# Performance work log

Hardware: AMD Instinct MI355X
Metric: run time of the kernel (lower is better)

Reference implementation:

```python
import jax, jax.numpy as jnp
import numpy as np

P = 2048  # number of problems


def _structure():
    # Symbols per problem alternate 128/384; questions per problem alternate 32/96.
    p = np.arange(P)
    S = np.where(p % 2 == 0, 128, 384).astype(np.int64)   # num_symbols per problem
    Q = np.where(p % 2 == 0, 32, 96).astype(np.int64)     # num_questions per problem
    cost_starts = np.concatenate([[0], np.cumsum(S)])[:-1]  # row starts into costs_flat
    prob_of_question = np.repeat(p, Q)                     # [T_Q] problem id of each question
    S_per_q = np.repeat(S, Q)                              # [T_Q] symbols per question
    TQ = S_per_q.shape[0]
    qs_segment = np.repeat(np.arange(TQ), S_per_q)         # [T_total] question id of each element
    q_elem_starts = np.concatenate([[0], np.cumsum(S_per_q)])[:-1]
    T = qs_segment.shape[0]
    # offset of each element within its question, then add that problem's cost row start
    offsets = np.arange(T) - np.repeat(q_elem_starts, S_per_q)
    starts_per_q = np.repeat(cost_starts, Q)
    cost_index = np.repeat(starts_per_q, S_per_q) + offsets  # tile_like gather indices
    return (cost_index.astype(np.int32), qs_segment.astype(np.int32),
            prob_of_question.astype(np.int32))


def setup_inputs() -> dict:
    key = jax.random.key(0)
    k1, k2, k3 = jax.random.split(key, 3)
    cost_index, qs_segment, prob_of_question = _structure()
    T = cost_index.shape[0]            # 41_943_040
    TS = (P // 2) * (128 + 384)        # 524_288
    occ_flat = jax.random.uniform(k1, (T,), dtype=jnp.float32)   # occurrence counts >= 0
    costs_flat = jax.random.normal(k2, (TS,), dtype=jnp.float32)  # symbol costs (weights)
    valid = jax.random.uniform(k3, (P,)) < 0.9                    # per-problem valid mask
    return {
        'occ_flat': occ_flat,
        'costs_flat': costs_flat,
        'valid': valid,
        'cost_index': jnp.asarray(cost_index),
        'qs_segment': jnp.asarray(qs_segment),
        'prob_of_question': jnp.asarray(prob_of_question),
    }


def reference(occ_flat, costs_flat, valid, cost_index, qs_segment, prob_of_question):
    # tile_like: broadcast each problem's costs to each of its questions (gather)
    # costs_to_logits: elementwise multiply + per-question reduce_sum
    # costs_decorated_to_logits: invalid problems' logits are 0 (scatter_nd into zeros)
    TQ = prob_of_question.shape[0]
    potentials = occ_flat * costs_flat[cost_index]             # [T_total]
    logits_q = jax.ops.segment_sum(potentials, qs_segment, num_segments=TQ)  # [T_Q]
    return jnp.where(valid[prob_of_question], logits_q, jnp.zeros((), logits_q.dtype))
```

## Files before the change

kernel.cpp:

```cpp
#include <hip/hip_runtime.h>
#include <hip/hip_bf16.h>


typedef float f4 __attribute__((ext_vector_type(4)));

__device__ __forceinline__ float dot4(f4 a, f4 b) {
    return a.x * b.x + a.y * b.y + a.z * b.z + a.w * b.w;
}

#define TQ_HALF 65536

__global__ __launch_bounds__(256)
void classifier_kernel(const float* __restrict__ occ,
                       const float* __restrict__ costs,
                       const void*  __restrict__ valid,
                       float* __restrict__ out) {
    const int hid   = (blockIdx.x * blockDim.x + threadIdx.x) >> 5;
    const int lane  = threadIdx.x & 31;
    const int flane = threadIdx.x & 63;

    unsigned int w = ((const unsigned int*)valid)[flane];
    const bool u8 = (__ballot(w > 1u) != 0ull);

    const int pair   = hid >> 7;
    const int within = hid & 127;
    const int pair2  = pair + (TQ_HALF >> 7);

    float s0, s1;
    int prob0, prob1;
    if (within < 32) {
        prob0 = 2 * pair;
        prob1 = 2 * pair2;
        const f4* o0 = (const f4*)(occ + 40960 * pair  + 128 * within);
        const f4* o1 = (const f4*)(occ + 40960 * pair2 + 128 * within);
        const f4* c0 = (const f4*)(costs + 512 * pair);
        const f4* c1 = (const f4*)(costs + 512 * pair2);
        f4 a0 = __builtin_nontemporal_load(&o0[lane]);
        f4 a1 = __builtin_nontemporal_load(&o1[lane]);
        f4 b0 = c0[lane];
        f4 b1 = c1[lane];
        s0 = dot4(a0, b0);
        s1 = dot4(a1, b1);
    } else {
        prob0 = 2 * pair + 1;
        prob1 = 2 * pair2 + 1;
        const f4* o0 = (const f4*)(occ + 40960 * pair  + 4096 + 384 * (within - 32));
        const f4* o1 = (const f4*)(occ + 40960 * pair2 + 4096 + 384 * (within - 32));
        const f4* c0 = (const f4*)(costs + 512 * pair  + 128);
        const f4* c1 = (const f4*)(costs + 512 * pair2 + 128);
        f4 a00 = __builtin_nontemporal_load(&o0[lane]);
        f4 a01 = __builtin_nontemporal_load(&o0[lane + 32]);
        f4 a02 = __builtin_nontemporal_load(&o0[lane + 64]);
        f4 a10 = __builtin_nontemporal_load(&o1[lane]);
        f4 a11 = __builtin_nontemporal_load(&o1[lane + 32]);
        f4 a12 = __builtin_nontemporal_load(&o1[lane + 64]);
        f4 b00 = c0[lane];
        f4 b01 = c0[lane + 32];
        f4 b02 = c0[lane + 64];
        f4 b10 = c1[lane];
        f4 b11 = c1[lane + 32];
        f4 b12 = c1[lane + 64];
        s0 = dot4(a00, b00) + dot4(a01, b01) + dot4(a02, b02);
        s1 = dot4(a10, b10) + dot4(a11, b11) + dot4(a12, b12);
    }

    #pragma unroll
    for (int off = 16; off > 0; off >>= 1) {
        s0 += __shfl_down(s0, off, 32);
        s1 += __shfl_down(s1, off, 32);
    }

    if (lane == 0) {
        bool v0 = u8 ? (((const unsigned char*)valid)[prob0] != 0)
                     : (((const int*)valid)[prob0] != 0);
        bool v1 = u8 ? (((const unsigned char*)valid)[prob1] != 0)
                     : (((const int*)valid)[prob1] != 0);
        out[hid]           = v0 ? s0 : 0.0f;
        out[hid + TQ_HALF] = v1 ? s1 : 0.0f;
    }
}

extern "C" void kernel_launch(void* const* d_in, const int* in_sizes, int n_in,
                              void* d_out, int out_size, void* d_ws, size_t ws_size,
                              hipStream_t stream) {
    const float* occ   = (const float*)d_in[0];
    const float* costs = (const float*)d_in[1];
    const void*  valid = (const void*)d_in[2];

    const int TQ      = out_size;
    const int threads = (TQ / 2) * 32;
    const int block   = 256;
    const int grid    = threads / block;

    classifier_kernel<<<grid, block, 0, stream>>>(occ, costs, valid, (float*)d_out);
}
```

Before: 352.8 us.

## Skip occ loads for invalid problems and regroup questions per problem

Each half-wave now handles two questions of the same problem instead of two problems half the array apart, so the cost vector is loaded once and reused for both dot products. The valid flag is checked before the loads, so invalid problems (about 10%) skip reading their large occ slices and just write zeros. The block-to-pair mapping interleaves pairs across blocks to spread memory traffic. This relies on the output being zero for invalid problems, which the reference requires, so the skipped reads are legitimately unnecessary.

```diff
diff --git a/kernel.cpp b/kernel.cpp
--- a/kernel.cpp
+++ b/kernel.cpp
@@ -1,5 +1,4 @@
 #include <hip/hip_runtime.h>
-#include <hip/hip_bf16.h>
 
 
 typedef float f4 __attribute__((ext_vector_type(4)));
@@ -8,60 +7,66 @@
     return a.x * b.x + a.y * b.y + a.z * b.z + a.w * b.w;
 }
 
-#define TQ_HALF 65536
-
 __global__ __launch_bounds__(256)
 void classifier_kernel(const float* __restrict__ occ,
                        const float* __restrict__ costs,
                        const void*  __restrict__ valid,
                        float* __restrict__ out) {
-    const int hid   = (blockIdx.x * blockDim.x + threadIdx.x) >> 5;
     const int lane  = threadIdx.x & 31;
     const int flane = threadIdx.x & 63;
 
     unsigned int w = ((const unsigned int*)valid)[flane];
     const bool u8 = (__ballot(w > 1u) != 0ull);
 
-    const int pair   = hid >> 7;
-    const int within = hid & 127;
-    const int pair2  = pair + (TQ_HALF >> 7);
+    const int g    = blockIdx.x;
+    const int pair = ((g >> 6) << 3) | (g & 7);
+    const int sub  = (g >> 3) & 7;
+    const int k    = (sub << 3) | (int)(threadIdx.x >> 5);
 
-    float s0, s1;
-    int prob0, prob1;
-    if (within < 32) {
-        prob0 = 2 * pair;
-        prob1 = 2 * pair2;
-        const f4* o0 = (const f4*)(occ + 40960 * pair  + 128 * within);
-        const f4* o1 = (const f4*)(occ + 40960 * pair2 + 128 * within);
-        const f4* c0 = (const f4*)(costs + 512 * pair);
-        const f4* c1 = (const f4*)(costs + 512 * pair2);
-        f4 a0 = __builtin_nontemporal_load(&o0[lane]);
-        f4 a1 = __builtin_nontemporal_load(&o1[lane]);
-        f4 b0 = c0[lane];
-        f4 b1 = c1[lane];
-        s0 = dot4(a0, b0);
-        s1 = dot4(a1, b1);
+    const float* pbase = occ + 40960 * pair;
+
+    float s0 = 0.0f, s1 = 0.0f;
+    int qa, qb;
+    if (k < 16) {
+        const int j = k;
+        qa = 128 * pair + j;
+        qb = qa + 16;
+        const int prob = 2 * pair;
+        const bool v = u8 ? (((const unsigned char*)valid)[prob] != 0)
+                          : (((const int*)valid)[prob] != 0);
+        if (v) {
+            const f4* o0 = (const f4*)(pbase + 128 * j);
+            const f4* o1 = (const f4*)(pbase + 128 * (j + 16));
+            const f4* c  = (const f4*)(costs + 512 * pair);
+            f4 a0 = __builtin_nontemporal_load(&o0[lane]);
+            f4 a1 = __builtin_nontemporal_load(&o1[lane]);
+            f4 b  = c[lane];
+            s0 = dot4(a0, b);
+            s1 = dot4(a1, b);
+        }
     } else {
-        prob0 = 2 * pair + 1;
-        prob1 = 2 * pair2 + 1;
-        const f4* o0 = (const f4*)(occ + 40960 * pair  + 4096 + 384 * (within - 32));
-        const f4* o1 = (const f4*)(occ + 40960 * pair2 + 4096 + 384 * (within - 32));
-        const f4* c0 = (const f4*)(costs + 512 * pair  + 128);
-        const f4* c1 = (const f4*)(costs + 512 * pair2 + 128);
-        f4 a00 = __builtin_nontemporal_load(&o0[lane]);
-        f4 a01 = __builtin_nontemporal_load(&o0[lane + 32]);
-        f4 a02 = __builtin_nontemporal_load(&o0[lane + 64]);
-        f4 a10 = __builtin_nontemporal_load(&o1[lane]);
-        f4 a11 = __builtin_nontemporal_load(&o1[lane + 32]);
-        f4 a12 = __builtin_nontemporal_load(&o1[lane + 64]);
-        f4 b00 = c0[lane];
-        f4 b01 = c0[lane + 32];
-        f4 b02 = c0[lane + 64];
-        f4 b10 = c1[lane];
-        f4 b11 = c1[lane + 32];
-        f4 b12 = c1[lane + 64];
-        s0 = dot4(a00, b00) + dot4(a01, b01) + dot4(a02, b02);
-        s1 = dot4(a10, b10) + dot4(a11, b11) + dot4(a12, b12);
+        const int j = k - 16;
+        qa = 128 * pair + 32 + j;
+        qb = qa + 48;
+        const int prob = 2 * pair + 1;
+        const bool v = u8 ? (((const unsigned char*)valid)[prob] != 0)
+                          : (((const int*)valid)[prob] != 0);
+        if (v) {
+            const f4* o0 = (const f4*)(pbase + 4096 + 384 * j);
+            const f4* o1 = (const f4*)(pbase + 4096 + 384 * (j + 48));
+            const f4* c  = (const f4*)(costs + 512 * pair + 128);
+            f4 a00 = __builtin_nontemporal_load(&o0[lane]);
+            f4 a01 = __builtin_nontemporal_load(&o0[lane + 32]);
+            f4 a02 = __builtin_nontemporal_load(&o0[lane + 64]);
+            f4 a10 = __builtin_nontemporal_load(&o1[lane]);
+            f4 a11 = __builtin_nontemporal_load(&o1[lane + 32]);
+            f4 a12 = __builtin_nontemporal_load(&o1[lane + 64]);
+            f4 b0  = c[lane];
+            f4 b1  = c[lane + 32];
+            f4 b2  = c[lane + 64];
+            s0 = dot4(a00, b0) + dot4(a01, b1) + dot4(a02, b2);
+            s1 = dot4(a10, b0) + dot4(a11, b1) + dot4(a12, b2);
+        }
     }
 
     #pragma unroll
@@ -71,12 +76,8 @@
     }
 
     if (lane == 0) {
-        bool v0 = u8 ? (((const unsigned char*)valid)[prob0] != 0)
-                     : (((const int*)valid)[prob0] != 0);
-        bool v1 = u8 ? (((const unsigned char*)valid)[prob1] != 0)
-                     : (((const int*)valid)[prob1] != 0);
-        out[hid]           = v0 ? s0 : 0.0f;
-        out[hid + TQ_HALF] = v1 ? s1 : 0.0f;
+        out[qa] = s0;
+        out[qb] = s1;
     }
 }
 
```

Measured after the change: 344.5 us. 1.02x faster.
